# Kernel optimization log

Hardware: AMD Instinct MI355X
Metric: run time of the kernel (lower is better)

The kernel has to match this reference:

```python
import jax, jax.numpy as jnp
import numpy as np

B, DIN, H1, H2 = 16384, 512, 256, 128
S, DC, DE, T, TE, GH = 4, 4, 2, 3, 2, 64
NDOM = DC * DE            # 8 domain experts total
ETOT = S + NDOM + TE      # 14 experts feeding each task gate


def setup_inputs() -> dict:
    key = jax.random.key(0)
    ks = jax.random.split(key, 20)
    w = lambda k, shape, fan: (jax.random.normal(k, shape, jnp.float32) / np.sqrt(fan).astype(np.float32))
    x = jax.random.normal(ks[0], (B, DIN), jnp.float32)
    domain_ids = jax.random.randint(ks[1], (B,), 0, DC, jnp.int64) if jax.config.jax_enable_x64 else jax.random.randint(ks[1], (B,), 0, DC, jnp.int32)
    return {
        "x": x,
        "domain_ids": domain_ids,
        # shared experts (stacked): input->256->128, ReLU on both layers
        "sW1": w(ks[2], (S, DIN, H1), DIN), "sb1": jnp.zeros((S, H1), jnp.float32),
        "sW2": w(ks[3], (S, H1, H2), H1),   "sb2": jnp.zeros((S, H2), jnp.float32),
        # domain experts, all domains stacked in order domain0..domainDC-1
        "dW1": w(ks[4], (NDOM, DIN, H1), DIN), "db1": jnp.zeros((NDOM, H1), jnp.float32),
        "dW2": w(ks[5], (NDOM, H1, H2), H1),   "db2": jnp.zeros((NDOM, H2), jnp.float32),
        # task experts, all tasks stacked task0..taskT-1
        "tW1": w(ks[6], (T * TE, DIN, H1), DIN), "tb1": jnp.zeros((T * TE, H1), jnp.float32),
        "tW2": w(ks[7], (T * TE, H1, H2), H1),   "tb2": jnp.zeros((T * TE, H2), jnp.float32),
        # task gates (stacked over tasks): input->64 (ReLU) -> ETOT (linear) -> softmax
        "gW1": w(ks[8], (T, DIN, GH), DIN), "gb1": jnp.zeros((T, GH), jnp.float32),
        "gW2": w(ks[9], (T, GH, ETOT), GH), "gb2": jnp.zeros((T, ETOT), jnp.float32),
    }


def _experts(x, W1, b1, W2, b2):
    # x: [B, DIN]; W1: [E, DIN, H1]; W2: [E, H1, H2] -> [B, E, H2]
    h = jax.nn.relu(jnp.einsum('bi,eih->beh', x, W1) + b1)
    return jax.nn.relu(jnp.einsum('beh,eho->beo', h, W2) + b2)


def reference(x, domain_ids, sW1, sb1, sW2, sb2, dW1, db1, dW2, db2,
              tW1, tb1, tW2, tb2, gW1, gb1, gW2, gb2):
    shared = _experts(x, sW1, sb1, sW2, sb2)          # [B, S, H2]
    domain = _experts(x, dW1, db1, dW2, db2)          # [B, NDOM, H2]
    task = _experts(x, tW1, tb1, tW2, tb2)            # [B, T*TE, H2]
    task = task.reshape(B, T, TE, H2)
    base = jnp.concatenate([shared, domain], axis=1)  # [B, S+NDOM, H2]
    base = jnp.broadcast_to(base[:, None], (B, T, S + NDOM, H2))
    all_experts = jnp.concatenate([base, task], axis=2)  # [B, T, ETOT, H2]
    # task gates
    gh = jax.nn.relu(jnp.einsum('bi,tig->btg', x, gW1) + gb1)
    gates = jax.nn.softmax(jnp.einsum('btg,tge->bte', gh, gW2) + gb2, axis=-1)  # [B, T, ETOT]
    out = jnp.einsum('bteh,bte->tbh', all_experts, gates)  # [T, B, H2]
    # note: the torch per-sample domain_weighted_output is computed then discarded;
    # only these task outputs are returned, and they do not depend on domain_ids.
    return tuple(out[t] for t in range(T))
```

## Files before the change

kernel.cpp:

```cpp
#include <hip/hip_runtime.h>
#include <hip/hip_bf16.h>

#define NB 16384
#define DIN 512
#define H1 256
#define H2 128
#define NE 18
#define NT 3
#define NGH 64
#define NETOT 14

typedef float f32x4 __attribute__((ext_vector_type(4)));
typedef short s16x8 __attribute__((ext_vector_type(8)));
typedef unsigned short u16;
typedef unsigned int u32;

__device__ __forceinline__ u16 f2bf(float f) {
    union { float f; u32 u; } v; v.f = f;
    u32 r = v.u + 0x7fffu + ((v.u >> 16) & 1u);
    return (u16)(r >> 16);
}
__device__ __forceinline__ float bf2f(u16 u) {
    union { u32 u; float f; } v; v.u = ((u32)u) << 16;
    return v.f;
}
__device__ __forceinline__ u32 cvtpk(float a, float b) {
    u32 r;
    asm("v_cvt_pk_bf16_f32 %0, %1, %2" : "=v"(r) : "v"(a), "v"(b));
    return r;
}

#define GLDS16(g, l) __builtin_amdgcn_global_load_lds((const u32*)(g), (u32*)(l), 16, 0, 0)

__global__ __launch_bounds__(256) void k_prep(
    const float* __restrict__ x, u16* __restrict__ xb,
    const float* __restrict__ sW1, const float* __restrict__ dW1, const float* __restrict__ tW1,
    const float* __restrict__ sW2, const float* __restrict__ dW2, const float* __restrict__ tW2,
    const float* __restrict__ gW1, u16* __restrict__ w1t, u16* __restrict__ w2t, u16* __restrict__ gw1t)
{
    __shared__ float lds[64 * 65];
    int bx = blockIdx.x;
    if (bx < 8192) {
        int i = (bx * 256 + threadIdx.x) * 4;
        float4 v = *reinterpret_cast<const float4*>(x + i);
        ushort4 o;
        o.x = f2bf(v.x); o.y = f2bf(v.y); o.z = f2bf(v.z); o.w = f2bf(v.w);
        *reinterpret_cast<ushort4*>(xb + i) = o;
        return;
    }
    int b = bx - 8192;
    const float* src; u16* dst; int K, N, k0, n0;
    if (b < 576) {
        int e = b >> 5, tile = b & 31;
        src = (e < 4) ? sW1 + (size_t)e * DIN * H1 : (e < 12) ? dW1 + (size_t)(e - 4) * DIN * H1
                                                              : tW1 + (size_t)(e - 12) * DIN * H1;
        dst = w1t + (size_t)e * H1 * DIN; K = DIN; N = H1;
        k0 = (tile >> 2) * 64; n0 = (tile & 3) * 64;
    } else if (b < 720) {
        int b2 = b - 576; int e = b2 >> 3, tile = b2 & 7;
        src = (e < 4) ? sW2 + (size_t)e * H1 * H2 : (e < 12) ? dW2 + (size_t)(e - 4) * H1 * H2
                                                             : tW2 + (size_t)(e - 12) * H1 * H2;
        dst = w2t + (size_t)e * H2 * H1; K = H1; N = H2;
        k0 = (tile >> 1) * 64; n0 = (tile & 1) * 64;
    } else {
        int b3 = b - 720; int t = b3 >> 3, tile = b3 & 7;
        src = gW1 + (size_t)t * DIN * NGH; dst = gw1t + (size_t)t * NGH * DIN; K = DIN; N = NGH;
        k0 = tile * 64; n0 = 0;
    }
    int t = threadIdx.x;
#pragma unroll
    for (int i = 0; i < 16; ++i) {
        int idx = i * 256 + t;
        int kk = idx >> 6, nn = idx & 63;
        lds[kk * 65 + nn] = src[(size_t)(k0 + kk) * N + n0 + nn];
    }
    __syncthreads();
#pragma unroll
    for (int i = 0; i < 16; ++i) {
        int idx = i * 256 + t;
        int nn = idx >> 6, kk = idx & 63;
        dst[(size_t)(n0 + nn) * K + k0 + kk] = f2bf(lds[kk * 65 + nn]);
    }
}

__global__ __launch_bounds__(256, 4) void k_expert_gate(
    const u16* __restrict__ xb, const u16* __restrict__ w1t, const u16* __restrict__ w2t,
    const float* __restrict__ sb1, const float* __restrict__ db1, const float* __restrict__ tb1,
    const float* __restrict__ sb2, const float* __restrict__ db2, const float* __restrict__ tb2,
    u16* __restrict__ eout,
    const u16* __restrict__ gw1t, const float* __restrict__ gb1,
    const float* __restrict__ gw2, const float* __restrict__ gb2, float* __restrict__ gates)
{
    __shared__ __align__(128) char smem[40960];

    const int bid = blockIdx.x;
    const int tid = threadIdx.x;

    if (bid >= 4608) {
        u16* xs  = reinterpret_cast<u16*>(smem);
        u16* g1s = reinterpret_cast<u16*>(smem) + 4608;
        u16* ghs = reinterpret_cast<u16*>(smem);

        int m0 = (bid - 4608) * 64;
        int w = tid >> 6, lane = tid & 63;
        int wm = w & 1, wn = w >> 1;
        int l15 = lane & 15, lk = (lane >> 4) * 8, lr4 = (lane >> 4) * 4;

        f32x4 acc[2][6];
#pragma unroll
        for (int i = 0; i < 2; ++i)
#pragma unroll
            for (int j = 0; j < 6; ++j) acc[i][j] = (f32x4)0.f;

        const u16* xg = xb + (size_t)m0 * DIN;
        int srow = tid >> 3, su = (tid & 7) * 8;
        for (int kc = 0; kc < DIN / 64; ++kc) {
#pragma unroll
            for (int it = 0; it < 2; ++it) {
                int rr = srow + it * 32;
                *reinterpret_cast<uint4*>(&xs[rr * 72 + su]) =
                    *reinterpret_cast<const uint4*>(xg + (size_t)rr * DIN + kc * 64 + su);
            }
#pragma unroll
            for (int it = 0; it < 6; ++it) {
                int rr = srow + it * 32;
                *reinterpret_cast<uint4*>(&g1s[rr * 72 + su]) =
                    *reinterpret_cast<const uint4*>(gw1t + (size_t)rr * DIN + kc * 64 + su);
            }
            __syncthreads();
            s16x8 af[2][2], bfr[6][2];
#pragma unroll
            for (int mi = 0; mi < 2; ++mi)
#pragma unroll
                for (int kk = 0; kk < 2; ++kk)
                    af[mi][kk] = *reinterpret_cast<const s16x8*>(&xs[(wm * 32 + mi * 16 + l15) * 72 + kk * 32 + lk]);
#pragma unroll
            for (int nj = 0; nj < 6; ++nj)
#pragma unroll
                for (int kk = 0; kk < 2; ++kk)
                    bfr[nj][kk] = *reinterpret_cast<const s16x8*>(&g1s[(wn * 96 + nj * 16 + l15) * 72 + kk * 32 + lk]);
#pragma unroll
            for (int kk = 0; kk < 2; ++kk)
#pragma unroll
                for (int mi = 0; mi < 2; ++mi)
#pragma unroll
                    for (int nj = 0; nj < 6; ++nj)
                        acc[mi][nj] = __builtin_amdgcn_mfma_f32_16x16x32_bf16(af[mi][kk], bfr[nj][kk], acc[mi][nj], 0, 0, 0);
            __syncthreads();
        }
#pragma unroll
        for (int mi = 0; mi < 2; ++mi)
#pragma unroll
            for (int nj = 0; nj < 6; ++nj) {
                int col = wn * 96 + nj * 16 + l15;
                float bias = gb1[col];
#pragma unroll
                for (int r = 0; r < 4; ++r) {
                    int row = wm * 32 + mi * 16 + lr4 + r;
                    float v = acc[mi][nj][r] + bias;
                    ghs[row * 200 + col] = f2bf(v > 0.f ? v : 0.f);
                }
            }
        __syncthreads();

        if (tid < 192) {
            int tt = tid >> 6, rr = tid & 63;
            float logit[NETOT];
#pragma unroll
            for (int e2 = 0; e2 < NETOT; ++e2) logit[e2] = gb2[tt * NETOT + e2];
            const float* g2 = gw2 + tt * NGH * NETOT;
            const u16* gr = &ghs[rr * 200 + tt * 64];
            for (int g = 0; g < NGH; ++g) {
                float v = bf2f(gr[g]);
#pragma unroll
                for (int e2 = 0; e2 < NETOT; ++e2) logit[e2] += v * g2[g * NETOT + e2];
            }
            float m = logit[0];
#pragma unroll
            for (int e2 = 1; e2 < NETOT; ++e2) m = fmaxf(m, logit[e2]);
            float s = 0.f, p[NETOT];
#pragma unroll
            for (int e2 = 0; e2 < NETOT; ++e2) { p[e2] = __expf(logit[e2] - m); s += p[e2]; }
            float inv = 1.f / s;
            float* go = gates + (size_t)(m0 + rr) * (NT * NETOT) + tt * NETOT;
#pragma unroll
            for (int e2 = 0; e2 < NETOT; ++e2) go[e2] = p[e2] * inv;
        }
        return;
    }

    const int e  = bid >> 8;
    const int m0 = (bid & 255) * 64;
    const int w = tid >> 6, lane = tid & 63;
    const int l15 = lane & 15, q = lane >> 4;
    const int q16 = q * 16;
    const int swk = ((l15 >> 1) & 3) << 4;

    const u16* xg  = xb + (size_t)m0 * DIN;
    const u16* w1g = w1t + (size_t)e * H1 * DIN;
    const u16* w2g = w2t + (size_t)e * H2 * H1;
    const float* b1p = (e < 4) ? sb1 + e * H1 : (e < 12) ? db1 + (e - 4) * H1 : tb1 + (e - 12) * H1;
    const float* b2p = (e < 4) ? sb2 + e * H2 : (e < 12) ? db2 + (e - 4) * H2 : tb2 + (e - 12) * H2;

    const int sr = lane >> 2, sc = lane & 3;
    const int xrow = w * 16 + sr;
    const u16* gx = xg + (size_t)xrow * DIN + ((sc ^ ((xrow >> 1) & 3)) * 8);
    const int lx = w * 1024;
    const u16* gw1[4]; int lw1[4];
#pragma unroll
    for (int j = 0; j < 4; ++j) {
        int row = w * 64 + j * 16 + sr;
        gw1[j] = w1g + (size_t)row * DIN + ((sc ^ ((row >> 1) & 3)) * 8);
        lw1[j] = 4096 + w * 4096 + j * 1024;
    }

    int offX[4], offW[4];
#pragma unroll
    for (int mi = 0; mi < 4; ++mi)
        offX[mi] = (mi * 16 + l15) * 64 + (q16 ^ swk);
#pragma unroll
    for (int nj = 0; nj < 4; ++nj)
        offW[nj] = 4096 + (w * 64 + nj * 16 + l15) * 64 + (q16 ^ swk);

    f32x4 acc1[4][4];
#pragma unroll
    for (int i = 0; i < 4; ++i)
#pragma unroll
        for (int j = 0; j < 4; ++j) acc1[i][j] = (f32x4)0.f;

    GLDS16(gx, smem + lx);
#pragma unroll
    for (int j = 0; j < 4; ++j) GLDS16(gw1[j], smem + lw1[j]);

    for (int kt = 0; kt < 16; ++kt) {
        if (kt < 15) {
            const int nb = ((kt + 1) & 1) * 20480, ko = (kt + 1) * 32;
            GLDS16(gx + ko, smem + nb + lx);
#pragma unroll
            for (int j = 0; j < 4; ++j) GLDS16(gw1[j] + ko, smem + nb + lw1[j]);
            asm volatile("s_waitcnt vmcnt(5)" ::: "memory");
        } else {
            asm volatile("s_waitcnt vmcnt(0)" ::: "memory");
        }
        __builtin_amdgcn_s_barrier();

        const char* cb = smem + (kt & 1) * 20480;
        s16x8 xf[4], wf[4];
#pragma unroll
        for (int nj = 0; nj < 4; ++nj) wf[nj] = *(const s16x8*)(cb + offW[nj]);
#pragma unroll
        for (int mi = 0; mi < 4; ++mi) xf[mi] = *(const s16x8*)(cb + offX[mi]);
        __builtin_amdgcn_s_setprio(1);
#pragma unroll
        for (int mi = 0; mi < 4; ++mi)
#pragma unroll
            for (int nj = 0; nj < 4; ++nj)
                acc1[mi][nj] = __builtin_amdgcn_mfma_f32_16x16x32_bf16(wf[nj], xf[mi], acc1[mi][nj], 0, 0, 0);
        __builtin_amdgcn_s_setprio(0);
        asm volatile("s_waitcnt lgkmcnt(0)" ::: "memory");
        __builtin_amdgcn_s_barrier();
    }

#pragma unroll
    for (int mi = 0; mi < 4; ++mi) {
        const int m = mi * 16 + l15;
        char* rowp = smem + m * 528;
#pragma unroll
        for (int nj = 0; nj < 4; ++nj) {
            const int n0 = w * 64 + nj * 16 + q * 4;
            const float4 bv = *reinterpret_cast<const float4*>(b1p + n0);
            float v0 = fmaxf(acc1[mi][nj][0] + bv.x, 0.f);
            float v1 = fmaxf(acc1[mi][nj][1] + bv.y, 0.f);
            float v2 = fmaxf(acc1[mi][nj][2] + bv.z, 0.f);
            float v3 = fmaxf(acc1[mi][nj][3] + bv.w, 0.f);
            uint2 hv; hv.x = cvtpk(v0, v1); hv.y = cvtpk(v2, v3);
            *reinterpret_cast<uint2*>(rowp + n0 * 2) = hv;
        }
    }
    __syncthreads();

    f32x4 acc2[4][2];
#pragma unroll
    for (int i = 0; i < 4; ++i)
#pragma unroll
        for (int j = 0; j < 2; ++j) acc2[i][j] = (f32x4)0.f;
    const u16* w2p0 = w2g + (size_t)(w * 32 + l15) * H1 + q * 8;
    const u16* w2p1 = w2g + (size_t)(w * 32 + 16 + l15) * H1 + q * 8;
#pragma unroll
    for (int kt2 = 0; kt2 < 8; ++kt2) {
        s16x8 wf2[2], hf[4];
        wf2[0] = *(const s16x8*)(w2p0 + kt2 * 32);
        wf2[1] = *(const s16x8*)(w2p1 + kt2 * 32);
#pragma unroll
        for (int mi = 0; mi < 4; ++mi)
            hf[mi] = *(const s16x8*)(smem + (mi * 16 + l15) * 528 + kt2 * 64 + q16);
#pragma unroll
        for (int mi = 0; mi < 4; ++mi)
#pragma unroll
            for (int pj = 0; pj < 2; ++pj)
                acc2[mi][pj] = __builtin_amdgcn_mfma_f32_16x16x32_bf16(hf[mi], wf2[pj], acc2[mi][pj], 0, 0, 0);
    }

    u16* eo = eout + ((size_t)e * NB + m0) * H2;
#pragma unroll
    for (int mi = 0; mi < 4; ++mi)
#pragma unroll
        for (int pj = 0; pj < 2; ++pj) {
            const int p = w * 32 + pj * 16 + l15;
            const float bias = b2p[p];
#pragma unroll
            for (int r = 0; r < 4; ++r) {
                const int row = mi * 16 + q * 4 + r;
                float v = acc2[mi][pj][r] + bias;
                eo[(size_t)row * H2 + p] = f2bf(v > 0.f ? v : 0.f);
            }
        }
}

__global__ __launch_bounds__(256) void k_combine(
    const u16* __restrict__ eout, const float* __restrict__ gates, float* __restrict__ out)
{
    int tid = threadIdx.x;
    int lr = tid >> 5, hq = tid & 31;
    int b = blockIdx.x * 8 + lr;
    int h0 = hq * 4;
    const float* g = gates + (size_t)b * (NT * NETOT);
    float o0[4] = {0, 0, 0, 0}, o1[4] = {0, 0, 0, 0}, o2[4] = {0, 0, 0, 0};
#pragma unroll
    for (int e = 0; e < NE; ++e) {
        ushort4 ev = *reinterpret_cast<const ushort4*>(&eout[((size_t)e * NB + b) * H2 + h0]);
        float v0 = bf2f(ev.x), v1 = bf2f(ev.y), v2 = bf2f(ev.z), v3 = bf2f(ev.w);
        if (e < 12) {
            float wa = g[e], wb = g[NETOT + e], wc = g[2 * NETOT + e];
            o0[0] += wa * v0; o0[1] += wa * v1; o0[2] += wa * v2; o0[3] += wa * v3;
            o1[0] += wb * v0; o1[1] += wb * v1; o1[2] += wb * v2; o1[3] += wb * v3;
            o2[0] += wc * v0; o2[1] += wc * v1; o2[2] += wc * v2; o2[3] += wc * v3;
        } else {
            int t = (e - 12) >> 1, te = (e - 12) & 1;
            float wt = g[t * NETOT + 12 + te];
            float* ot = (t == 0) ? o0 : (t == 1) ? o1 : o2;
            ot[0] += wt * v0; ot[1] += wt * v1; ot[2] += wt * v2; ot[3] += wt * v3;
        }
    }
    size_t base = (size_t)b * H2 + h0;
    *reinterpret_cast<float4*>(&out[0 * (size_t)NB * H2 + base]) = make_float4(o0[0], o0[1], o0[2], o0[3]);
    *reinterpret_cast<float4*>(&out[1 * (size_t)NB * H2 + base]) = make_float4(o1[0], o1[1], o1[2], o1[3]);
    *reinterpret_cast<float4*>(&out[2 * (size_t)NB * H2 + base]) = make_float4(o2[0], o2[1], o2[2], o2[3]);
}

extern "C" void kernel_launch(void* const* d_in, const int* in_sizes, int n_in,
                              void* d_out, int out_size, void* d_ws, size_t ws_size,
                              hipStream_t stream)
{
    const float* x   = (const float*)d_in[0];
    const float* sW1 = (const float*)d_in[2];
    const float* sb1 = (const float*)d_in[3];
    const float* sW2 = (const float*)d_in[4];
    const float* sb2 = (const float*)d_in[5];
    const float* dW1 = (const float*)d_in[6];
    const float* db1 = (const float*)d_in[7];
    const float* dW2 = (const float*)d_in[8];
    const float* db2 = (const float*)d_in[9];
    const float* tW1 = (const float*)d_in[10];
    const float* tb1 = (const float*)d_in[11];
    const float* tW2 = (const float*)d_in[12];
    const float* tb2 = (const float*)d_in[13];
    const float* gW1 = (const float*)d_in[14];
    const float* gb1 = (const float*)d_in[15];
    const float* gW2 = (const float*)d_in[16];
    const float* gb2 = (const float*)d_in[17];

    char* ws = (char*)d_ws;
    u16*  xb    = (u16*)(ws + 0);
    u16*  w1t   = (u16*)(ws + 16777216);
    u16*  w2t   = (u16*)(ws + 21495808);
    u16*  gw1t  = (u16*)(ws + 22675456);
    float* gates = (float*)(ws + 22872064);
    u16*  eout  = (u16*)(ws + 25624576);

    k_prep<<<dim3(8936), dim3(256), 0, stream>>>(x, xb, sW1, dW1, tW1, sW2, dW2, tW2, gW1, w1t, w2t, gw1t);
    k_expert_gate<<<dim3(4864), dim3(256), 0, stream>>>(xb, w1t, w2t, sb1, db1, tb1, sb2, db2, tb2,
                                                        eout, gw1t, gb1, gW2, gb2, gates);
    k_combine<<<dim3(NB / 8), dim3(256), 0, stream>>>(eout, gates, (float*)d_out);
}
```

Baseline: 176.1 us.

## Use 128-row expert tiles, 512-thread blocks, and a three-stage load pipeline

The expert kernel moves from 64-row, 256-thread tiles to 128-row, 512-thread tiles arranged as a 2x4 wave grid. This halves the weight re-reads per sample row. The first-layer K loop now uses a three-buffer ring with prefetch two steps ahead, which removes the trailing barrier in each iteration. The gate path keeps its hidden activations in fp32 in shared memory, and only four of its eight waves run the MFMA work. The cost is a larger LDS footprint (72KB) and lower per-CU block occupancy.

```diff
diff --git a/kernel.cpp b/kernel.cpp
--- a/kernel.cpp
+++ b/kernel.cpp
@@ -83,7 +83,7 @@
     }
 }
 
-__global__ __launch_bounds__(256, 4) void k_expert_gate(
+__global__ __launch_bounds__(512, 2) void k_expert_gate(
     const u16* __restrict__ xb, const u16* __restrict__ w1t, const u16* __restrict__ w2t,
     const float* __restrict__ sb1, const float* __restrict__ db1, const float* __restrict__ tb1,
     const float* __restrict__ sb2, const float* __restrict__ db2, const float* __restrict__ tb2,
@@ -91,20 +91,22 @@
     const u16* __restrict__ gw1t, const float* __restrict__ gb1,
     const float* __restrict__ gw2, const float* __restrict__ gb2, float* __restrict__ gates)
 {
-    __shared__ __align__(128) char smem[40960];
+    __shared__ __align__(128) char smem[73728];
 
     const int bid = blockIdx.x;
     const int tid = threadIdx.x;
-
-    if (bid >= 4608) {
+    const int w = tid >> 6, lane = tid & 63;
+    const int l15 = lane & 15, q = lane >> 4;
+    const int q16 = q * 16;
+
+    if (bid >= 2304) {
         u16* xs  = reinterpret_cast<u16*>(smem);
         u16* g1s = reinterpret_cast<u16*>(smem) + 4608;
-        u16* ghs = reinterpret_cast<u16*>(smem);
-
-        int m0 = (bid - 4608) * 64;
-        int w = tid >> 6, lane = tid & 63;
-        int wm = w & 1, wn = w >> 1;
-        int l15 = lane & 15, lk = (lane >> 4) * 8, lr4 = (lane >> 4) * 4;
+        float* ghs = reinterpret_cast<float*>(smem);
+
+        int m0 = (bid - 2304) * 64;
+        int wm = w & 1, wn = (w >> 1) & 1;
+        int lk = q * 8, lr4 = q * 4;
 
         f32x4 acc[2][6];
 #pragma unroll
@@ -113,54 +115,54 @@
             for (int j = 0; j < 6; ++j) acc[i][j] = (f32x4)0.f;
 
         const u16* xg = xb + (size_t)m0 * DIN;
-        int srow = tid >> 3, su = (tid & 7) * 8;
+        const int srow = tid >> 3, su = (tid & 7) * 8;
         for (int kc = 0; kc < DIN / 64; ++kc) {
-#pragma unroll
-            for (int it = 0; it < 2; ++it) {
-                int rr = srow + it * 32;
-                *reinterpret_cast<uint4*>(&xs[rr * 72 + su]) =
-                    *reinterpret_cast<const uint4*>(xg + (size_t)rr * DIN + kc * 64 + su);
-            }
-#pragma unroll
-            for (int it = 0; it < 6; ++it) {
-                int rr = srow + it * 32;
+            *reinterpret_cast<uint4*>(&xs[srow * 72 + su]) =
+                *reinterpret_cast<const uint4*>(xg + (size_t)srow * DIN + kc * 64 + su);
+#pragma unroll
+            for (int it = 0; it < 3; ++it) {
+                int rr = it * 64 + srow;
                 *reinterpret_cast<uint4*>(&g1s[rr * 72 + su]) =
                     *reinterpret_cast<const uint4*>(gw1t + (size_t)rr * DIN + kc * 64 + su);
             }
             __syncthreads();
-            s16x8 af[2][2], bfr[6][2];
+            if (w < 4) {
+                s16x8 af[2][2], bfr[6][2];
+#pragma unroll
+                for (int mi = 0; mi < 2; ++mi)
+#pragma unroll
+                    for (int kk = 0; kk < 2; ++kk)
+                        af[mi][kk] = *reinterpret_cast<const s16x8*>(&xs[(wm * 32 + mi * 16 + l15) * 72 + kk * 32 + lk]);
+#pragma unroll
+                for (int nj = 0; nj < 6; ++nj)
+#pragma unroll
+                    for (int kk = 0; kk < 2; ++kk)
+                        bfr[nj][kk] = *reinterpret_cast<const s16x8*>(&g1s[(wn * 96 + nj * 16 + l15) * 72 + kk * 32 + lk]);
+#pragma unroll
+                for (int kk = 0; kk < 2; ++kk)
+#pragma unroll
+                    for (int mi = 0; mi < 2; ++mi)
+#pragma unroll
+                        for (int nj = 0; nj < 6; ++nj)
+                            acc[mi][nj] = __builtin_amdgcn_mfma_f32_16x16x32_bf16(af[mi][kk], bfr[nj][kk], acc[mi][nj], 0, 0, 0);
+            }
+            __syncthreads();
+        }
+        if (w < 4) {
 #pragma unroll
             for (int mi = 0; mi < 2; ++mi)
 #pragma unroll
-                for (int kk = 0; kk < 2; ++kk)
-                    af[mi][kk] = *reinterpret_cast<const s16x8*>(&xs[(wm * 32 + mi * 16 + l15) * 72 + kk * 32 + lk]);
-#pragma unroll
-            for (int nj = 0; nj < 6; ++nj)
-#pragma unroll
-                for (int kk = 0; kk < 2; ++kk)
-                    bfr[nj][kk] = *reinterpret_cast<const s16x8*>(&g1s[(wn * 96 + nj * 16 + l15) * 72 + kk * 32 + lk]);
-#pragma unroll
-            for (int kk = 0; kk < 2; ++kk)
-#pragma unroll
-                for (int mi = 0; mi < 2; ++mi)
-#pragma unroll
-                    for (int nj = 0; nj < 6; ++nj)
-                        acc[mi][nj] = __builtin_amdgcn_mfma_f32_16x16x32_bf16(af[mi][kk], bfr[nj][kk], acc[mi][nj], 0, 0, 0);
-            __syncthreads();
-        }
-#pragma unroll
-        for (int mi = 0; mi < 2; ++mi)
-#pragma unroll
-            for (int nj = 0; nj < 6; ++nj) {
-                int col = wn * 96 + nj * 16 + l15;
-                float bias = gb1[col];
-#pragma unroll
-                for (int r = 0; r < 4; ++r) {
-                    int row = wm * 32 + mi * 16 + lr4 + r;
-                    float v = acc[mi][nj][r] + bias;
-                    ghs[row * 200 + col] = f2bf(v > 0.f ? v : 0.f);
+                for (int nj = 0; nj < 6; ++nj) {
+                    int col = wn * 96 + nj * 16 + l15;
+                    float bias = gb1[col];
+#pragma unroll
+                    for (int r = 0; r < 4; ++r) {
+                        int row = wm * 32 + mi * 16 + lr4 + r;
+                        float v = acc[mi][nj][r] + bias;
+                        ghs[row * 200 + col] = v > 0.f ? v : 0.f;
+                    }
                 }
-            }
+        }
         __syncthreads();
 
         if (tid < 192) {
@@ -169,9 +171,9 @@
 #pragma unroll
             for (int e2 = 0; e2 < NETOT; ++e2) logit[e2] = gb2[tt * NETOT + e2];
             const float* g2 = gw2 + tt * NGH * NETOT;
-            const u16* gr = &ghs[rr * 200 + tt * 64];
+            const float* gr = &ghs[rr * 200 + tt * 64];
             for (int g = 0; g < NGH; ++g) {
-                float v = bf2f(gr[g]);
+                float v = gr[g];
 #pragma unroll
                 for (int e2 = 0; e2 < NETOT; ++e2) logit[e2] += v * g2[g * NETOT + e2];
             }
@@ -189,12 +191,9 @@
         return;
     }
 
-    const int e  = bid >> 8;
-    const int m0 = (bid & 255) * 64;
-    const int w = tid >> 6, lane = tid & 63;
-    const int l15 = lane & 15, q = lane >> 4;
-    const int q16 = q * 16;
-    const int swk = ((l15 >> 1) & 3) << 4;
+    const int e  = bid >> 7;
+    const int m0 = (bid & 127) * 128;
+    const int wm = w & 1, wn = w >> 1;
 
     const u16* xg  = xb + (size_t)m0 * DIN;
     const u16* w1g = w1t + (size_t)e * H1 * DIN;
@@ -206,21 +205,25 @@
     const int xrow = w * 16 + sr;
     const u16* gx = xg + (size_t)xrow * DIN + ((sc ^ ((xrow >> 1) & 3)) * 8);
     const int lx = w * 1024;
-    const u16* gw1[4]; int lw1[4];
-#pragma unroll
-    for (int j = 0; j < 4; ++j) {
-        int row = w * 64 + j * 16 + sr;
+    const u16* gw1[2]; int lw1[2];
+#pragma unroll
+    for (int j = 0; j < 2; ++j) {
+        int row = w * 32 + j * 16 + sr;
         gw1[j] = w1g + (size_t)row * DIN + ((sc ^ ((row >> 1) & 3)) * 8);
-        lw1[j] = 4096 + w * 4096 + j * 1024;
+        lw1[j] = 8192 + w * 2048 + j * 1024;
     }
 
     int offX[4], offW[4];
 #pragma unroll
-    for (int mi = 0; mi < 4; ++mi)
-        offX[mi] = (mi * 16 + l15) * 64 + (q16 ^ swk);
-#pragma unroll
-    for (int nj = 0; nj < 4; ++nj)
-        offW[nj] = 4096 + (w * 64 + nj * 16 + l15) * 64 + (q16 ^ swk);
+    for (int mi = 0; mi < 4; ++mi) {
+        int r = wm * 64 + mi * 16 + l15;
+        offX[mi] = r * 64 + (q16 ^ (((r >> 1) & 3) << 4));
+    }
+#pragma unroll
+    for (int nj = 0; nj < 4; ++nj) {
+        int n = wn * 64 + nj * 16 + l15;
+        offW[nj] = 8192 + n * 64 + (q16 ^ (((n >> 1) & 3) << 4));
+    }
 
     f32x4 acc1[4][4];
 #pragma unroll
@@ -230,21 +233,28 @@
 
     GLDS16(gx, smem + lx);
 #pragma unroll
-    for (int j = 0; j < 4; ++j) GLDS16(gw1[j], smem + lw1[j]);
-
+    for (int j = 0; j < 2; ++j) GLDS16(gw1[j], smem + lw1[j]);
+    GLDS16(gx + 32, smem + 24576 + lx);
+#pragma unroll
+    for (int j = 0; j < 2; ++j) GLDS16(gw1[j] + 32, smem + 24576 + lw1[j]);
+
+    int cur = 0, stg = 2;
     for (int kt = 0; kt < 16; ++kt) {
         if (kt < 15) {
-            const int nb = ((kt + 1) & 1) * 20480, ko = (kt + 1) * 32;
-            GLDS16(gx + ko, smem + nb + lx);
-#pragma unroll
-            for (int j = 0; j < 4; ++j) GLDS16(gw1[j] + ko, smem + nb + lw1[j]);
-            asm volatile("s_waitcnt vmcnt(5)" ::: "memory");
+            asm volatile("s_waitcnt vmcnt(3)" ::: "memory");
         } else {
             asm volatile("s_waitcnt vmcnt(0)" ::: "memory");
         }
         __builtin_amdgcn_s_barrier();
 
-        const char* cb = smem + (kt & 1) * 20480;
+        if (kt < 14) {
+            const int sb = stg * 24576, ko = (kt + 2) * 32;
+            GLDS16(gx + ko, smem + sb + lx);
+#pragma unroll
+            for (int j = 0; j < 2; ++j) GLDS16(gw1[j] + ko, smem + sb + lw1[j]);
+        }
+
+        const char* cb = smem + cur * 24576;
         s16x8 xf[4], wf[4];
 #pragma unroll
         for (int nj = 0; nj < 4; ++nj) wf[nj] = *(const s16x8*)(cb + offW[nj]);
@@ -257,17 +267,19 @@
             for (int nj = 0; nj < 4; ++nj)
                 acc1[mi][nj] = __builtin_amdgcn_mfma_f32_16x16x32_bf16(wf[nj], xf[mi], acc1[mi][nj], 0, 0, 0);
         __builtin_amdgcn_s_setprio(0);
-        asm volatile("s_waitcnt lgkmcnt(0)" ::: "memory");
-        __builtin_amdgcn_s_barrier();
-    }
+
+        cur = (cur == 2) ? 0 : cur + 1;
+        stg = (stg == 2) ? 0 : stg + 1;
+    }
+    __syncthreads();
 
 #pragma unroll
     for (int mi = 0; mi < 4; ++mi) {
-        const int m = mi * 16 + l15;
+        const int m = wm * 64 + mi * 16 + l15;
         char* rowp = smem + m * 528;
 #pragma unroll
         for (int nj = 0; nj < 4; ++nj) {
-            const int n0 = w * 64 + nj * 16 + q * 4;
+            const int n0 = wn * 64 + nj * 16 + q * 4;
             const float4 bv = *reinterpret_cast<const float4*>(b1p + n0);
             float v0 = fmaxf(acc1[mi][nj][0] + bv.x, 0.f);
             float v1 = fmaxf(acc1[mi][nj][1] + bv.y, 0.f);
@@ -284,8 +296,8 @@
     for (int i = 0; i < 4; ++i)
 #pragma unroll
         for (int j = 0; j < 2; ++j) acc2[i][j] = (f32x4)0.f;
-    const u16* w2p0 = w2g + (size_t)(w * 32 + l15) * H1 + q * 8;
-    const u16* w2p1 = w2g + (size_t)(w * 32 + 16 + l15) * H1 + q * 8;
+    const u16* w2p0 = w2g + (size_t)(wn * 32 + l15) * H1 + q * 8;
+    const u16* w2p1 = w2g + (size_t)(wn * 32 + 16 + l15) * H1 + q * 8;
 #pragma unroll
     for (int kt2 = 0; kt2 < 8; ++kt2) {
         s16x8 wf2[2], hf[4];
@@ -293,7 +305,7 @@
         wf2[1] = *(const s16x8*)(w2p1 + kt2 * 32);
 #pragma unroll
         for (int mi = 0; mi < 4; ++mi)
-            hf[mi] = *(const s16x8*)(smem + (mi * 16 + l15) * 528 + kt2 * 64 + q16);
+            hf[mi] = *(const s16x8*)(smem + (wm * 64 + mi * 16 + l15) * 528 + kt2 * 64 + q16);
 #pragma unroll
         for (int mi = 0; mi < 4; ++mi)
 #pragma unroll
@@ -306,11 +318,11 @@
     for (int mi = 0; mi < 4; ++mi)
 #pragma unroll
         for (int pj = 0; pj < 2; ++pj) {
-            const int p = w * 32 + pj * 16 + l15;
+            const int p = wn * 32 + pj * 16 + l15;
             const float bias = b2p[p];
 #pragma unroll
             for (int r = 0; r < 4; ++r) {
-                const int row = mi * 16 + q * 4 + r;
+                const int row = wm * 64 + mi * 16 + q * 4 + r;
                 float v = acc2[mi][pj][r] + bias;
                 eo[(size_t)row * H2 + p] = f2bf(v > 0.f ? v : 0.f);
             }
@@ -379,7 +391,7 @@
     u16*  eout  = (u16*)(ws + 25624576);
 
     k_prep<<<dim3(8936), dim3(256), 0, stream>>>(x, xb, sW1, dW1, tW1, sW2, dW2, tW2, gW1, w1t, w2t, gw1t);
-    k_expert_gate<<<dim3(4864), dim3(256), 0, stream>>>(xb, w1t, w2t, sb1, db1, tb1, sb2, db2, tb2,
+    k_expert_gate<<<dim3(2560), dim3(512), 0, stream>>>(xb, w1t, w2t, sb1, db1, tb1, sb2, db2, tb2,
                                                         eout, gw1t, gb1, gW2, gb2, gates);
     k_combine<<<dim3(NB / 8), dim3(256), 0, stream>>>(eout, gates, (float*)d_out);
 }
```

Result: no change. 174.7 us (-0.8%).
